# Optimization experiments

Hardware: AMD Instinct MI355X
Metric: run time of the kernel (lower is better)

Reference implementation:

```python
import jax, jax.numpy as jnp
import numpy as np

N, D, L = 8192, 128, 5
EPS = 1e-5  # BatchNorm1d default eps
MRATIO, MSTD = 0.5, 0.5


def _prelu(x, a):
    return jnp.where(x >= 0, x, a * x)


def _gcn(x, adj, W, b, a):
    # x: [1,N,Din], adj: [1,N,N]; DGI-style GCN: act(adj @ (x W) + b)
    h = jnp.einsum('bnd,de->bne', x, W)
    out = jnp.einsum('bnm,bme->bne', adj, h) + b
    return _prelu(out, a)


def _bn(x2d, gamma, beta):
    # training-mode BatchNorm1d over the node axis, biased variance
    mu = jnp.mean(x2d, axis=0)
    var = jnp.mean((x2d - mu) ** 2, axis=0)
    return gamma * (x2d - mu) * jax.lax.rsqrt(var + EPS) + beta


def setup_inputs():
    key = jax.random.key(0)
    ks = jax.random.split(key, 6)
    x = jax.random.normal(ks[0], (1, N, D), jnp.float32)
    # dense normalized-ish adjacency; scale keeps row sums ~1
    adj = jax.random.uniform(ks[1], (1, N, N), jnp.float32) * (2.0 / N)
    # vectorized 'partial' masking: Bernoulli(mratio) element mask + N(0, mstd) noise
    mask = (jax.random.uniform(ks[2], (1, N, D)) < MRATIO).astype(jnp.float32)
    noise = jax.random.normal(ks[3], (1, N, D), jnp.float32) * MSTD

    def mk(k):
        kw, kg, kb = jax.random.split(k, 3)
        return dict(
            W=jax.random.normal(kw, (L, D, D), jnp.float32) / np.sqrt(D),
            b=jnp.zeros((L, D), jnp.float32),
            alpha=jnp.full((L,), 0.25, jnp.float32),  # PReLU default
            gamma=jax.random.uniform(kg, (L, D), jnp.float32, minval=0.5, maxval=1.5),
            beta=jax.random.normal(kb, (L, D), jnp.float32) * 0.1,
        )

    enc, dec = mk(ks[4]), mk(ks[5])
    return {
        'x': x, 'adj': adj, 'mask': mask, 'noise': noise,
        'enc_W': enc['W'], 'enc_b': enc['b'], 'enc_alpha': enc['alpha'],
        'enc_gamma': enc['gamma'], 'enc_beta': enc['beta'],
        'dec_W': dec['W'], 'dec_b': dec['b'], 'dec_alpha': dec['alpha'],
        'dec_gamma': dec['gamma'], 'dec_beta': dec['beta'],
    }


def reference(x, adj, mask, noise, enc_W, enc_b, enc_alpha, enc_gamma, enc_beta,
              dec_W, dec_b, dec_alpha, dec_gamma, dec_beta):
    # mask_node 'partial' (vectorized); torch mutates x in place, so x_embed == masked x
    x_m = x * (1.0 - mask) + noise * mask

    # Encoder: L x (GCN -> BN)
    h = x_m
    for i in range(L):
        h = _gcn(h, adj, enc_W[i], enc_b[i], enc_alpha[i])
        h = _bn(h[0], enc_gamma[i], enc_beta[i])[None]
    encoded = h

    # Decoder: L x GCN, BN except after last layer
    d = encoded
    for i in range(L):
        d = _gcn(d, adj, dec_W[i], dec_b[i], dec_alpha[i])
        if i < L - 1:
            d = _bn(d[0], dec_gamma[i], dec_beta[i])[None]

    return (x_m, encoded, d, mask)
```

## Files before the change

### kernel.cpp

```cpp
#include <hip/hip_runtime.h>
#include <hip/hip_bf16.h>
#include <stdint.h>

typedef unsigned short u16;
typedef unsigned int u32;

typedef __attribute__((__ext_vector_type__(8))) short short8;
typedef __attribute__((__ext_vector_type__(4))) float float4v;
typedef __attribute__((__ext_vector_type__(16))) float float16v;

typedef const u32 __attribute__((address_space(1))) gu32;
typedef u32 __attribute__((address_space(3))) lu32;

__device__ __forceinline__ u16 f2b(float f) {
  __hip_bfloat16 h = __float2bfloat16(f);
  return *reinterpret_cast<u16*>(&h);
}

__device__ __forceinline__ void gld16(const void* g, void* l) {
  __builtin_amdgcn_global_load_lds((gu32*)g, (lu32*)l, 16, 0, 0);
}

__global__ __launch_bounds__(256) void k_cvt(const float* __restrict__ a, u16* __restrict__ o) {
  int t = blockIdx.x * 256 + threadIdx.x;
  float4 v0 = ((const float4*)a)[2 * t];
  float4 v1 = ((const float4*)a)[2 * t + 1];
  u16 r[8];
  r[0] = f2b(v0.x); r[1] = f2b(v0.y); r[2] = f2b(v0.z); r[3] = f2b(v0.w);
  r[4] = f2b(v1.x); r[5] = f2b(v1.y); r[6] = f2b(v1.z); r[7] = f2b(v1.w);
  ((uint4*)o)[t] = *(const uint4*)r;
}

__global__ __launch_bounds__(256) void k_mask(
    const float* __restrict__ x, const float* __restrict__ msk, const float* __restrict__ nz,
    u16* __restrict__ H, float* __restrict__ oxm, float* __restrict__ omask, float* __restrict__ ST)
{
  int t = blockIdx.x * 256 + threadIdx.x;
  if (blockIdx.x == 0) {
#pragma unroll
    for (int k = 0; k < 10; ++k) ST[threadIdx.x + k * 256] = 0.f;
  }
  float xv[8], mv[8], nv[8], rv[8];
  *(float4*)&xv[0] = ((const float4*)x)[2 * t];
  *(float4*)&xv[4] = ((const float4*)x)[2 * t + 1];
  *(float4*)&mv[0] = ((const float4*)msk)[2 * t];
  *(float4*)&mv[4] = ((const float4*)msk)[2 * t + 1];
  *(float4*)&nv[0] = ((const float4*)nz)[2 * t];
  *(float4*)&nv[4] = ((const float4*)nz)[2 * t + 1];
  u16 res[8];
#pragma unroll
  for (int j = 0; j < 8; ++j) {
    rv[j] = xv[j] * (1.f - mv[j]) + nv[j] * mv[j];
    res[j] = f2b(rv[j]);
  }
  ((uint4*)H)[t] = *(const uint4*)res;
  ((float4*)oxm)[2 * t]     = *(const float4*)&rv[0];
  ((float4*)oxm)[2 * t + 1] = *(const float4*)&rv[4];
  ((float4*)omask)[2 * t]     = *(const float4*)&mv[0];
  ((float4*)omask)[2 * t + 1] = *(const float4*)&mv[4];
}

template <int MODE>
__global__ __launch_bounds__(256) void k_mm1(
    const u16* __restrict__ Hin, const float* __restrict__ ACTt,
    const float* __restrict__ STp, const float* __restrict__ gamma, const float* __restrict__ beta,
    const float* __restrict__ W, u16* __restrict__ Tc, float* __restrict__ oenc)
{
  __shared__ __align__(16) u16 Wl[128 * 136];
  __shared__ __align__(16) u16 Hl[128 * 136];
  const int tid = threadIdx.x;
  const int w = tid >> 6, lane = tid & 63;
  const int ln = lane & 15, quad = lane >> 4;
  const int i0 = blockIdx.x * 128;

#pragma unroll
  for (int it = 0; it < 16; ++it) {
    int idx4 = (it * 256 + tid) * 4;
    int e = idx4 >> 7, d0 = idx4 & 127;
    float4 v = *(const float4*)(W + idx4);
    Wl[(d0 + 0) * 136 + e] = f2b(v.x);
    Wl[(d0 + 1) * 136 + e] = f2b(v.y);
    Wl[(d0 + 2) * 136 + e] = f2b(v.z);
    Wl[(d0 + 3) * 136 + e] = f2b(v.w);
  }
  if (MODE == 0) {
#pragma unroll
    for (int it = 0; it < 8; ++it) {
      int chunk = tid + it * 256;
      int r = chunk >> 4, c8 = (chunk & 15) * 8;
      uint4 v = *(const uint4*)(Hin + (size_t)(i0 + r) * 128 + c8);
      *(uint4*)(&Hl[r * 136 + c8]) = v;
    }
  } else {
#pragma unroll
    for (int it = 0; it < 8; ++it) {
      int tmp = it * 256 + tid;
      int e = tmp >> 4, i8 = (tmp & 15) * 8;
      float mu = STp[e] * (1.f / 8192.f);
      float var = STp[128 + e] * (1.f / 8192.f) - mu * mu;
      float sc = gamma[e] * rsqrtf(var + 1e-5f);
      float sh = beta[e] - mu * sc;
      const float* src = ACTt + (size_t)e * 8192 + i0 + i8;
      float4 v0 = *(const float4*)src;
      float4 v1 = *(const float4*)(src + 4);
      float r[8] = {v0.x, v0.y, v0.z, v0.w, v1.x, v1.y, v1.z, v1.w};
#pragma unroll
      for (int j = 0; j < 8; ++j) {
        r[j] = r[j] * sc + sh;
        Hl[(i8 + j) * 136 + e] = f2b(r[j]);
      }
      if (MODE == 2) {
#pragma unroll
        for (int j = 0; j < 8; ++j) oenc[(size_t)(i0 + i8 + j) * 128 + e] = r[j];
      }
    }
  }
  __syncthreads();

  float4v acc[2][8] = {};
#pragma unroll
  for (int ks = 0; ks < 4; ++ks) {
    short8 a[2], b[8];
#pragma unroll
    for (int r = 0; r < 2; ++r)
      a[r] = *(const short8*)&Wl[(w * 32 + r * 16 + ln) * 136 + ks * 32 + quad * 8];
#pragma unroll
    for (int c = 0; c < 8; ++c)
      b[c] = *(const short8*)&Hl[(c * 16 + ln) * 136 + ks * 32 + quad * 8];
#pragma unroll
    for (int r = 0; r < 2; ++r)
#pragma unroll
      for (int c = 0; c < 8; ++c)
        acc[r][c] = __builtin_amdgcn_mfma_f32_16x16x32_bf16(a[r], b[c], acc[r][c], 0, 0, 0);
  }
#pragma unroll
  for (int r = 0; r < 2; ++r)
#pragma unroll
    for (int c = 0; c < 8; ++c)
#pragma unroll
      for (int g = 0; g < 4; ++g) {
        int d = w * 32 + r * 16 + quad * 4 + g;
        int i = i0 + c * 16 + ln;
        Tc[((size_t)(i >> 3) * 128 + d) * 8 + (i & 7)] = f2b(acc[r][c][g]);
      }
}

__global__ __launch_bounds__(256, 1) void k_gemm(
    const u16* __restrict__ adjB, const u16* __restrict__ Tc, float* __restrict__ PB)
{
  __shared__ __align__(16) u16 Al[2][32 * 128 * 8];
  const int tid = threadIdx.x;
  const int w = tid >> 6, lane = tid & 63;
  const int lrow = lane & 31, lhalf = lane >> 5;
  const int wd = w >> 1, wi = w & 1;
  const int nt = blockIdx.x >> 2, seg = blockIdx.x & 3;
  const int i0 = nt * 128;

  const u16* bp0 = adjB + (size_t)(i0 + wi * 64 + lrow) * 8192 + seg * 2048 + lhalf * 8;
  const u16* bp1 = bp0 + (size_t)32 * 8192;

  float16v acc[2][2] = {};

  auto stage = [&](int p, int ss) {
    const u16* src = Tc + ((size_t)(seg * 256 + ss * 32) * 128 + tid) * 8;
    u16* dst = &Al[p][tid * 8];
#pragma unroll
    for (int c = 0; c < 16; ++c)
      gld16(src + c * 2048, dst + c * 2048);
  };

  auto compute = [&](int p) {
#pragma unroll 4
    for (int t = 0; t < 16; ++t) {
      short8 b0 = *(const short8*)(bp0 + t * 16);
      short8 b1 = *(const short8*)(bp1 + t * 16);
      short8 a0 = *(const short8*)&Al[p][((t * 2 + lhalf) * 128 + wd * 64 + lrow) * 8];
      short8 a1 = *(const short8*)&Al[p][((t * 2 + lhalf) * 128 + wd * 64 + 32 + lrow) * 8];
      acc[0][0] = __builtin_amdgcn_mfma_f32_32x32x16_bf16(a0, b0, acc[0][0], 0, 0, 0);
      acc[0][1] = __builtin_amdgcn_mfma_f32_32x32x16_bf16(a0, b1, acc[0][1], 0, 0, 0);
      acc[1][0] = __builtin_amdgcn_mfma_f32_32x32x16_bf16(a1, b0, acc[1][0], 0, 0, 0);
      acc[1][1] = __builtin_amdgcn_mfma_f32_32x32x16_bf16(a1, b1, acc[1][1], 0, 0, 0);
    }
    bp0 += 256; bp1 += 256;
  };

  stage(0, 0);
  __syncthreads();
#pragma unroll
  for (int ss = 0; ss < 8; ++ss) {
    if (ss < 7) stage((ss & 1) ^ 1, ss + 1);
    compute(ss & 1);
    __syncthreads();
  }

  const int ib = i0 + wi * 64 + lrow;
#pragma unroll
  for (int dm = 0; dm < 2; ++dm)
#pragma unroll
    for (int nb = 0; nb < 2; ++nb)
#pragma unroll
      for (int g = 0; g < 16; ++g) {
        int d = wd * 64 + dm * 32 + (g & 3) + 8 * (g >> 2) + 4 * lhalf;
        PB[((size_t)seg * 128 + d) * 8192 + ib + nb * 32] = acc[dm][nb][g];
      }
}

template <bool LAST>
__global__ __launch_bounds__(256) void k_red(
    const float* __restrict__ PB, const float* __restrict__ bias, const float* __restrict__ alphaP,
    float* __restrict__ ACTt, float* __restrict__ ST, float* __restrict__ outL)
{
  const int d = blockIdx.x >> 1, half = blockIdx.x & 1;
  const int tid = threadIdx.x;
  const float bb = bias[d], alpha = alphaP[0];
  const float* pb = PB + (size_t)d * 8192 + half * 4096;
  float s1 = 0.f, s2 = 0.f;
#pragma unroll
  for (int it = 0; it < 4; ++it) {
    int idx = it * 1024 + tid * 4;
    float4 v = *(const float4*)(pb + idx);
#pragma unroll
    for (int s = 1; s < 4; ++s) {
      float4 u = *(const float4*)(pb + (size_t)s * 1048576 + idx);
      v.x += u.x; v.y += u.y; v.z += u.z; v.w += u.w;
    }
    float r[4];
    const float* vp = (const float*)&v;
#pragma unroll
    for (int j = 0; j < 4; ++j) {
      float u = vp[j] + bb;
      r[j] = (u >= 0.f) ? u : alpha * u;
    }
    if (LAST) {
      int i = half * 4096 + idx;
#pragma unroll
      for (int j = 0; j < 4; ++j) outL[(size_t)(i + j) * 128 + d] = r[j];
    } else {
      *(float4*)(ACTt + (size_t)d * 8192 + half * 4096 + idx) = *(const float4*)r;
#pragma unroll
      for (int j = 0; j < 4; ++j) { s1 += r[j]; s2 += r[j] * r[j]; }
    }
  }
  if (!LAST) {
#pragma unroll
    for (int off = 1; off < 64; off <<= 1) {
      s1 += __shfl_xor(s1, off);
      s2 += __shfl_xor(s2, off);
    }
    __shared__ float red[8];
    if ((tid & 63) == 0) { red[(tid >> 6) * 2] = s1; red[(tid >> 6) * 2 + 1] = s2; }
    __syncthreads();
    if (tid == 0) {
      atomicAdd(ST + d, red[0] + red[2] + red[4] + red[6]);
      atomicAdd(ST + 128 + d, red[1] + red[3] + red[5] + red[7]);
    }
  }
}

extern "C" void kernel_launch(void* const* d_in, const int* in_sizes, int n_in,
                              void* d_out, int out_size, void* d_ws, size_t ws_size,
                              hipStream_t stream)
{
  const float* x     = (const float*)d_in[0];
  const float* adj   = (const float*)d_in[1];
  const float* msk   = (const float*)d_in[2];
  const float* nz    = (const float*)d_in[3];
  const float* encW  = (const float*)d_in[4];
  const float* encB  = (const float*)d_in[5];
  const float* encA  = (const float*)d_in[6];
  const float* encG  = (const float*)d_in[7];
  const float* encBe = (const float*)d_in[8];
  const float* decW  = (const float*)d_in[9];
  const float* decB  = (const float*)d_in[10];
  const float* decA  = (const float*)d_in[11];
  const float* decG  = (const float*)d_in[12];
  const float* decBe = (const float*)d_in[13];

  char* ws = (char*)d_ws;
  u16*   adjB = (u16*)ws;
  u16*   Tc   = (u16*)(ws + 134217728ull);
  u16*   H    = (u16*)(ws + 138412032ull);
  float* ACTt = (float*)(ws + 140509184ull);
  float* PB   = (float*)(ws + 144703488ull);
  float* ST   = (float*)(ws + 178257920ull);

  float* out   = (float*)d_out;
  float* o_xm  = out;
  float* o_enc = out + 1048576;
  float* o_dec = out + 2097152;
  float* o_msk = out + 3145728;

  k_cvt<<<32768, 256, 0, stream>>>(adj, adjB);
  k_mask<<<512, 256, 0, stream>>>(x, msk, nz, H, o_xm, o_msk, ST);

  for (int l = 0; l < 10; ++l) {
    bool e = l < 5;
    int li = e ? l : l - 5;
    const float* W  = (e ? encW : decW) + li * 16384;
    const float* bb = (e ? encB : decB) + li * 128;
    const float* al = (e ? encA : decA) + li;
    float* st = ST + l * 256;

    if (l == 0) {
      k_mm1<0><<<64, 256, 0, stream>>>(H, nullptr, nullptr, nullptr, nullptr, W, Tc, nullptr);
    } else {
      int pl = l - 1;
      bool pe = pl < 5;
      int pli = pe ? pl : pl - 5;
      const float* pg = (pe ? encG : decG) + pli * 128;
      const float* pbeta = (pe ? encBe : decBe) + pli * 128;
      const float* pst = ST + pl * 256;
      if (l == 5) k_mm1<2><<<64, 256, 0, stream>>>(nullptr, ACTt, pst, pg, pbeta, W, Tc, o_enc);
      else        k_mm1<1><<<64, 256, 0, stream>>>(nullptr, ACTt, pst, pg, pbeta, W, Tc, nullptr);
    }

    k_gemm<<<256, 256, 0, stream>>>(adjB, Tc, PB);

    if (l == 9) {
      k_red<true><<<256, 256, 0, stream>>>(PB, bb, al, nullptr, nullptr, o_dec);
    } else {
      k_red<false><<<256, 256, 0, stream>>>(PB, bb, al, ACTt, st, nullptr);
    }
  }
}
```

Measured before the change: 1.051 ms.

## Split adjacency GEMM K-dimension into eight segments with smaller LDS tiles

The adj@H GEMM now splits the K dimension into 8 segments instead of 4, doubling the grid to 512 blocks. Each block uses half the LDS, and each wave owns 32 rows across all 128 feature columns. Launch bounds now allow 2 blocks per CU, which should raise occupancy and latency hiding on the 256-CU part. In exchange, the partial-sum buffer PB doubles in size, the reduction kernel reads 8 partials instead of 4, and any PB allocation sized for only 4 segments would overflow.

```diff
diff --git a/kernel.cpp b/kernel.cpp
--- a/kernel.cpp
+++ b/kernel.cpp
@@ -145,43 +145,42 @@
       }
 }
 
-__global__ __launch_bounds__(256, 1) void k_gemm(
+__global__ __launch_bounds__(256, 2) void k_gemm(
     const u16* __restrict__ adjB, const u16* __restrict__ Tc, float* __restrict__ PB)
 {
-  __shared__ __align__(16) u16 Al[2][32 * 128 * 8];
+  __shared__ __align__(16) u16 Al[2][16 * 128 * 8];
   const int tid = threadIdx.x;
   const int w = tid >> 6, lane = tid & 63;
   const int lrow = lane & 31, lhalf = lane >> 5;
-  const int wd = w >> 1, wi = w & 1;
-  const int nt = blockIdx.x >> 2, seg = blockIdx.x & 3;
+  const int nt = blockIdx.x >> 3, seg = blockIdx.x & 7;
   const int i0 = nt * 128;
 
-  const u16* bp0 = adjB + (size_t)(i0 + wi * 64 + lrow) * 8192 + seg * 2048 + lhalf * 8;
-  const u16* bp1 = bp0 + (size_t)32 * 8192;
-
-  float16v acc[2][2] = {};
+  const u16* bp = adjB + (size_t)(i0 + w * 32 + lrow) * 8192 + seg * 1024 + lhalf * 8;
+
+  float16v acc[4] = {};
 
   auto stage = [&](int p, int ss) {
-    const u16* src = Tc + ((size_t)(seg * 256 + ss * 32) * 128 + tid) * 8;
+    const u16* src = Tc + ((size_t)(seg * 128 + ss * 16) * 128 + tid) * 8;
     u16* dst = &Al[p][tid * 8];
 #pragma unroll
-    for (int c = 0; c < 16; ++c)
+    for (int c = 0; c < 8; ++c)
       gld16(src + c * 2048, dst + c * 2048);
   };
 
   auto compute = [&](int p) {
-#pragma unroll 4
-    for (int t = 0; t < 16; ++t) {
-      short8 b0 = *(const short8*)(bp0 + t * 16);
-      short8 b1 = *(const short8*)(bp1 + t * 16);
-      short8 a0 = *(const short8*)&Al[p][((t * 2 + lhalf) * 128 + wd * 64 + lrow) * 8];
-      short8 a1 = *(const short8*)&Al[p][((t * 2 + lhalf) * 128 + wd * 64 + 32 + lrow) * 8];
-      acc[0][0] = __builtin_amdgcn_mfma_f32_32x32x16_bf16(a0, b0, acc[0][0], 0, 0, 0);
-      acc[0][1] = __builtin_amdgcn_mfma_f32_32x32x16_bf16(a0, b1, acc[0][1], 0, 0, 0);
-      acc[1][0] = __builtin_amdgcn_mfma_f32_32x32x16_bf16(a1, b0, acc[1][0], 0, 0, 0);
-      acc[1][1] = __builtin_amdgcn_mfma_f32_32x32x16_bf16(a1, b1, acc[1][1], 0, 0, 0);
-    }
-    bp0 += 256; bp1 += 256;
+#pragma unroll
+    for (int t = 0; t < 8; ++t) {
+      short8 b = *(const short8*)(bp + t * 16);
+      short8 a0 = *(const short8*)&Al[p][((t * 2 + lhalf) * 128 + lrow) * 8];
+      short8 a1 = *(const short8*)&Al[p][((t * 2 + lhalf) * 128 + 32 + lrow) * 8];
+      short8 a2 = *(const short8*)&Al[p][((t * 2 + lhalf) * 128 + 64 + lrow) * 8];
+      short8 a3 = *(const short8*)&Al[p][((t * 2 + lhalf) * 128 + 96 + lrow) * 8];
+      acc[0] = __builtin_amdgcn_mfma_f32_32x32x16_bf16(a0, b, acc[0], 0, 0, 0);
+      acc[1] = __builtin_amdgcn_mfma_f32_32x32x16_bf16(a1, b, acc[1], 0, 0, 0);
+      acc[2] = __builtin_amdgcn_mfma_f32_32x32x16_bf16(a2, b, acc[2], 0, 0, 0);
+      acc[3] = __builtin_amdgcn_mfma_f32_32x32x16_bf16(a3, b, acc[3], 0, 0, 0);
+    }
+    bp += 128;
   };
 
   stage(0, 0);
@@ -193,16 +192,14 @@
     __syncthreads();
   }
 
-  const int ib = i0 + wi * 64 + lrow;
-#pragma unroll
-  for (int dm = 0; dm < 2; ++dm)
-#pragma unroll
-    for (int nb = 0; nb < 2; ++nb)
-#pragma unroll
-      for (int g = 0; g < 16; ++g) {
-        int d = wd * 64 + dm * 32 + (g & 3) + 8 * (g >> 2) + 4 * lhalf;
-        PB[((size_t)seg * 128 + d) * 8192 + ib + nb * 32] = acc[dm][nb][g];
-      }
+  const int ib = i0 + w * 32 + lrow;
+#pragma unroll
+  for (int dm = 0; dm < 4; ++dm)
+#pragma unroll
+    for (int g = 0; g < 16; ++g) {
+      int d = dm * 32 + (g & 3) + 8 * (g >> 2) + 4 * lhalf;
+      PB[((size_t)seg * 128 + d) * 8192 + ib] = acc[dm][g];
+    }
 }
 
 template <bool LAST>
@@ -220,7 +217,7 @@
     int idx = it * 1024 + tid * 4;
     float4 v = *(const float4*)(pb + idx);
 #pragma unroll
-    for (int s = 1; s < 4; ++s) {
+    for (int s = 1; s < 8; ++s) {
       float4 u = *(const float4*)(pb + (size_t)s * 1048576 + idx);
       v.x += u.x; v.y += u.y; v.z += u.z; v.w += u.w;
     }
@@ -314,7 +311,7 @@
       else        k_mm1<1><<<64, 256, 0, stream>>>(nullptr, ACTt, pst, pg, pbeta, W, Tc, nullptr);
     }
 
-    k_gemm<<<256, 256, 0, stream>>>(adjB, Tc, PB);
+    k_gemm<<<512, 256, 0, stream>>>(adjB, Tc, PB);
 
     if (l == 9) {
       k_red<true><<<256, 256, 0, stream>>>(PB, bb, al, nullptr, nullptr, o_dec);
```

Result: faster. 934.7 us (-11.0%).
